# Optimization experiments

Hardware: AMD Instinct MI355X
Metric: run time of the kernel (lower is better)

Reference implementation:

```python
import jax, jax.numpy as jnp
import numpy as np

NUM_CODES = 128
BETA = 0.25


def conv1d(x, w, b):
    # x: (B, C, T), w: (O, I, K) torch layout, 'same' padding for k=3
    y = jax.lax.conv_general_dilated(x, w, window_strides=(1,), padding=[(1, 1)],
                                     dimension_numbers=('NCH', 'OIH', 'NCH'))
    return y + b[None, :, None]


def setup_inputs() -> dict:
    key = jax.random.key(0)
    ks = jax.random.split(key, 8)
    B, C, T, K = 16, 192, 8192, NUM_CODES
    fan = 1.0 / np.sqrt(C * 3)
    inp = {
        'x': jax.random.normal(ks[0], (B, C, T), jnp.float32),
        'enc_w1': jax.random.normal(ks[1], (C, C, 3), jnp.float32) * fan,
        'enc_b1': jnp.zeros((C,), jnp.float32),
        'enc_w2': jax.random.normal(ks[2], (C, C, 3), jnp.float32) * fan,
        'enc_b2': jnp.zeros((C,), jnp.float32),
        'emb': jax.random.normal(ks[3], (K, C), jnp.float32) * (1.0 / K),
        'dec_w1': jax.random.normal(ks[4], (C, C, 3), jnp.float32) * fan,
        'dec_b1': jnp.zeros((C,), jnp.float32),
        'dec_w2': jax.random.normal(ks[5], (C, C, 3), jnp.float32) * fan,
        'dec_b2': jnp.zeros((C,), jnp.float32),
        'dec_w3': jax.random.normal(ks[6], (C, C, 3), jnp.float32) * fan,
        'dec_b3': jnp.zeros((C,), jnp.float32),
    }
    return inp


def vector_quantize(z_e, emb):
    # z_e: (B, C, T) -> tokens (B*T, C)
    B, C, T = z_e.shape
    z = jnp.transpose(z_e, (0, 2, 1)).reshape(-1, C)          # (N, C)
    # squared distances ||z||^2 + ||e||^2 - 2 z.e
    d = (jnp.sum(z * z, axis=1, keepdims=True)
         + jnp.sum(emb * emb, axis=1)[None, :]
         - 2.0 * (z @ emb.T))                                  # (N, K)
    idx = jnp.argmin(d, axis=1)                                # (N,)
    z_q = emb[idx]                                             # (N, C) gather
    # loss = ||sg(z_q) - z||^2*... standard: codebook + beta*commitment
    loss = (jnp.mean((jax.lax.stop_gradient(z_q) - z) ** 2)
            + BETA * jnp.mean((z_q - jax.lax.stop_gradient(z)) ** 2))
    # perplexity of code usage
    n = z.shape[0]
    counts = jnp.zeros((emb.shape[0],), z.dtype).at[idx].add(1.0)
    probs = counts / n
    perplexity = jnp.exp(-jnp.sum(probs * jnp.log(probs + 1e-10)))
    # straight-through
    z_q = z + jax.lax.stop_gradient(z_q - z)
    z_q = jnp.transpose(z_q.reshape(B, T, C), (0, 2, 1))
    return loss, z_q, perplexity, idx


def reference(x, enc_w1, enc_b1, enc_w2, enc_b2, emb,
              dec_w1, dec_b1, dec_w2, dec_b2, dec_w3, dec_b3):
    # encoder: conv -> relu -> conv
    z_e = conv1d(jax.nn.relu(conv1d(x, enc_w1, enc_b1)), enc_w2, enc_b2)
    embedding_loss, z_q, perplexity, _ = vector_quantize(z_e, emb)
    # NOTE: source forward decodes z_e (not z_q) — reproduced faithfully
    h = jax.nn.relu(conv1d(z_e, dec_w1, dec_b1))
    h = jax.nn.relu(conv1d(h, dec_w2, dec_b2))
    x_hat = conv1d(h, dec_w3, dec_b3)
    return embedding_loss, x_hat, perplexity
```

## Files before the change

kernel.cpp:

```cpp
#include <hip/hip_runtime.h>
#include <hip/hip_bf16.h>
#include <stdint.h>

typedef short s16x8 __attribute__((ext_vector_type(8)));
typedef float f32x4 __attribute__((ext_vector_type(4)));
typedef unsigned int u32;
typedef unsigned short u16;

#define CCH 192
#define APITCH 200
#define NCODES 128
#define HALO 9
#define RPB 8216
#define LEAD 12
#define TOK 256
#define AROWS 274
#define CHS 16384

__device__ __forceinline__ u16 f2b(float f) {
  u32 u = __builtin_bit_cast(u32, f);
  u = (u + 0x7fffu + ((u >> 16) & 1u)) >> 16;
  return (u16)u;
}
__device__ __forceinline__ float b2f(u16 h) {
  return __builtin_bit_cast(float, ((u32)h) << 16);
}
__device__ __forceinline__ void gld16(const void* g, void* l) {
  __builtin_amdgcn_global_load_lds(
      (const __attribute__((address_space(1))) void*)g,
      (__attribute__((address_space(3))) void*)l, 16, 0, 0);
}

__global__ __launch_bounds__(256) void k_tin(const float* __restrict__ x, u16* __restrict__ xtp,
                                             int B, int T) {
  __shared__ float tile[32][36];
  int nt = T >> 5;
  int bid = blockIdx.x;
  int b = bid / (6 * nt);
  int rem = bid % (6 * nt);
  int cb = rem / nt, tb = rem % nt;
  int tid = threadIdx.x;
  {
    int c = tid >> 3, seg = tid & 7;
    const float* src = x + ((size_t)b * CCH + cb * 32 + c) * T + tb * 32 + seg * 4;
    float4 v = *(const float4*)src;
    tile[c][seg * 4 + 0] = v.x; tile[c][seg * 4 + 1] = v.y;
    tile[c][seg * 4 + 2] = v.z; tile[c][seg * 4 + 3] = v.w;
  }
  __syncthreads();
  {
    int t = tid >> 3, cs = tid & 7;
    u16* dst = xtp + ((size_t)(b * RPB + LEAD + tb * 32 + t)) * APITCH + cb * 32 + cs * 4;
    ushort4 o;
    o.x = f2b(tile[cs * 4 + 0][t]); o.y = f2b(tile[cs * 4 + 1][t]);
    o.z = f2b(tile[cs * 4 + 2][t]); o.w = f2b(tile[cs * 4 + 3][t]);
    *(ushort4*)dst = o;
  }
}

__global__ __launch_bounds__(256) void k_padz(u16* __restrict__ xtp) {
  int b = blockIdx.x;
  for (int i = threadIdx.x; i < 24 * 25; i += 256) {
    int r = i / 25, c = i - (i / 25) * 25;
    int row = (r < 12) ? r : (RPB - 12 + (r - 12));
    uint4 z = {0u, 0u, 0u, 0u};
    *(uint4*)((char*)xtp + ((size_t)(b * RPB + row)) * 400 + c * 16) = z;
  }
}

__global__ __launch_bounds__(256) void k_wconv(const float* __restrict__ w, u16* __restrict__ dst) {
  int i = blockIdx.x * 256 + threadIdx.x;
  if (i >= 3 * CCH * CCH) return;
  int cb = i / 18432;
  int r = i - cb * 18432;
  int k = r / 6144;
  int r2 = r - k * 6144;
  int o = r2 / 32, il = r2 - o * 32;
  dst[(size_t)(cb * 3 + k) * (CHS / 2) + (il >> 3) * 1536 + o * 8 + (il & 7)] =
      f2b(w[(o * CCH + cb * 32 + il) * 3 + k]);
}

__global__ __launch_bounds__(64) void k_emb(const float* __restrict__ emb, u16* __restrict__ embp,
                                            float* __restrict__ e2) {
  int code = blockIdx.x, lane = threadIdx.x;
  float s = 0.f;
  for (int j = lane * 3; j < lane * 3 + 3; ++j) {
    float v = emb[code * CCH + j];
    int cb = j >> 5, il = j & 31;
    embp[(size_t)cb * 4096 + (il >> 3) * 1024 + code * 8 + (il & 7)] = f2b(v);
    s += v * v;
  }
  #pragma unroll
  for (int m = 1; m < 64; m <<= 1) s += __shfl_xor(s, m, 64);
  if (lane == 0) e2[code] = s;
}

__global__ void k_zero(int* hist, double* dsum) {
  int t = threadIdx.x;
  if (t < NCODES) hist[t] = 0;
  if (t == 0) *dsum = 0.0;
}

__device__ __forceinline__ void issueW(const char* src, u16* dstb, int wv, int lane) {
  const char* s0 = src + wv * 2048 + lane * 16;
  char* d0 = (char*)dstb + wv * 2048 + lane * 16;
  gld16(s0, d0);
  gld16(s0 + 1024, d0 + 1024);
}
__device__ __forceinline__ void issueE(const char* src, u16* dstb, int tid) {
  gld16(src + tid * 16, (char*)dstb + tid * 16);
}

template<int F, int S, int M>
__device__ __forceinline__ void af_load(u32 aaddr, s16x8 (&a)[2][F]) {
  constexpr int cb = S / 3, k = S - 3 * (S / 3);
  constexpr int imm = (16 * M + k) * 400 + cb * 64;
  asm volatile("ds_read_b128 %0, %1 offset:%2" : "=v"(a[S & 1][M]) : "v"(aaddr), "i"(imm));
  if constexpr (M + 1 < F) af_load<F, S, M + 1>(aaddr, a);
}
template<int NF>
__device__ __forceinline__ void wf_load(u32 wq, s16x8 (&wf)[3]) {
  asm volatile("ds_read_b128 %0, %1 offset:%2" : "=v"(wf[NF]) : "v"(wq), "i"(NF * 256));
  if constexpr (NF + 1 < 3) wf_load<NF + 1>(wq, wf);
}

template<int G0, int F, int NEXT, int S>
__device__ __forceinline__ void cstep(const char* __restrict__ wtp, const char* __restrict__ embp,
                                      u16 (*wb)[8192], u32 aaddr, u32 wq0, u32 wq1,
                                      int wv, int lane, int tid,
                                      s16x8 (&a)[2][F], f32x4 (&acc)[F][3]) {
  asm volatile("s_waitcnt vmcnt(0)" ::: "memory");
  __builtin_amdgcn_sched_barrier(0);
  __builtin_amdgcn_s_barrier();
  if constexpr (S < 17) issueW(wtp + (size_t)(G0 + S + 1) * CHS, wb[(S + 1) & 1], wv, lane);
  else if constexpr (NEXT == 1) issueW(wtp + (size_t)(G0 + 18) * CHS, wb[0], wv, lane);
  else if constexpr (NEXT == 2) issueE(embp, wb[0], tid);
  if constexpr (S == 0) af_load<F, 0, 0>(aaddr, a);
  s16x8 wf[3];
  wf_load<0>((S & 1) ? wq1 : wq0, wf);
  if constexpr (S < 17) {
    af_load<F, S + 1, 0>(aaddr, a);
    if constexpr (F == 9) asm volatile("s_waitcnt lgkmcnt(9)" ::: "memory");
    else                  asm volatile("s_waitcnt lgkmcnt(8)" ::: "memory");
  } else {
    asm volatile("s_waitcnt lgkmcnt(0)" ::: "memory");
  }
  __builtin_amdgcn_sched_barrier(0);
  #pragma unroll
  for (int nf = 0; nf < 3; ++nf)
    #pragma unroll
    for (int m = 0; m < F; ++m)
      acc[m][nf] = __builtin_amdgcn_mfma_f32_16x16x32_bf16(a[S & 1][m], wf[nf], acc[m][nf], 0, 0, 0);
  if constexpr (S + 1 < 18)
    cstep<G0, F, NEXT, S + 1>(wtp, embp, wb, aaddr, wq0, wq1, wv, lane, tid, a, acc);
}

template<int G0, int F, int NEXT>
__device__ __forceinline__ void conv_phase(const char* __restrict__ wtp, const char* __restrict__ embp,
                                           u16 (*wb)[8192], u32 aaddr, u32 wq0, u32 wq1,
                                           int wv, int lane, int tid, f32x4 (&acc)[F][3]) {
  s16x8 a[2][F];
  cstep<G0, F, NEXT, 0>(wtp, embp, wb, aaddr, wq0, wq1, wv, lane, tid, a, acc);
}

template<int F, bool RELU>
__device__ __forceinline__ void writeback(u16* __restrict__ act, const f32x4 (&acc)[F][3],
                                          const float* bv, int oB, int lr, int lg, int rbase,
                                          int t0, int T, bool edge) {
  __builtin_amdgcn_s_barrier();
  if (!edge) {
    #pragma unroll
    for (int m = 0; m < F; ++m)
      #pragma unroll
      for (int nf = 0; nf < 3; ++nf) {
        int o = oB + nf * 16 + lr;
        #pragma unroll
        for (int r = 0; r < 4; ++r) {
          int row = rbase + 16 * m + lg * 4 + r;
          float v = acc[m][nf][r] + bv[nf];
          if (RELU) v = fmaxf(v, 0.f);
          act[row * APITCH + o] = f2b(v);
        }
      }
  } else {
    #pragma unroll
    for (int m = 0; m < F; ++m)
      #pragma unroll
      for (int nf = 0; nf < 3; ++nf) {
        int o = oB + nf * 16 + lr;
        #pragma unroll
        for (int r = 0; r < 4; ++r) {
          int row = rbase + 16 * m + lg * 4 + r;
          int tok = t0 - HALO + row;
          float v = acc[m][nf][r] + bv[nf];
          if (RELU) v = fmaxf(v, 0.f);
          if (tok < 0 || tok >= T) v = 0.f;
          act[row * APITCH + o] = f2b(v);
        }
      }
  }
  asm volatile("s_waitcnt lgkmcnt(0)" ::: "memory");
  __builtin_amdgcn_s_barrier();
}

__global__ __launch_bounds__(512, 1) void k_fused(
    const char* __restrict__ xtp, const char* __restrict__ wtp,
    const float* __restrict__ eb1, const float* __restrict__ eb2,
    const float* __restrict__ db1, const float* __restrict__ db2, const float* __restrict__ db3,
    const char* __restrict__ embp, const float* __restrict__ e2,
    int* __restrict__ hist, double* __restrict__ dsum,
    float* __restrict__ xhat, int T) {
  __shared__ __align__(16) u16 act[AROWS * APITCH];
  __shared__ __align__(16) u16 wb[2][8192];
  __shared__ int hs[NCODES];
  __shared__ float wsum[8];
  const int tid = threadIdx.x;
  const int wv = tid >> 6, lane = tid & 63, lr = lane & 15, lg = lane >> 4;
  const int nw = wv & 3, mw = wv >> 2;
  const int bid = blockIdx.x;
  const int b = bid >> 5, tile = bid & 31;
  const int t0 = tile * TOK;
  const bool edge = (tile == 0) || (tile == 31);
  const int oB = nw * 48;
  const int rbase = 1 + mw * 128;
  if (tid < NCODES) hs[tid] = 0;

  const u32 aaddr = (u32)(uintptr_t)act + (u32)(((rbase - 1 + lr) * APITCH + lg * 8) * 2);
  const u32 wq0 = (u32)(uintptr_t)wb[0] + (u32)((lg * 1536 + (oB + lr) * 8) * 2);
  const u32 wq1 = wq0 + 16384u;

  float bvv[5][3];
  #pragma unroll
  for (int nf = 0; nf < 3; ++nf) {
    int o = oB + nf * 16 + lr;
    bvv[0][nf] = eb1[o]; bvv[1][nf] = eb2[o];
    bvv[2][nf] = db1[o]; bvv[3][nf] = db2[o]; bvv[4][nf] = db3[o];
  }

  {
    const char* src = xtp + (size_t)(b * RPB + LEAD + t0 - HALO) * 400;
    #pragma unroll
    for (int s = 0; s < 14; ++s) {
      int c = tid + s * 512;
      if (c < AROWS * 25)
        gld16(src + (size_t)c * 16, (char*)act + (size_t)c * 16);
    }
  }
  issueW(wtp, wb[0], wv, lane);

  {
    f32x4 acc[9][3];
    #pragma unroll
    for (int m = 0; m < 9; ++m)
      #pragma unroll
      for (int n = 0; n < 3; ++n) acc[m][n] = f32x4{0.f, 0.f, 0.f, 0.f};
    conv_phase<0, 9, 1>(wtp, embp, wb, aaddr, wq0, wq1, wv, lane, tid, acc);
    writeback<9, true>(act, acc, bvv[0], oB, lr, lg, rbase, t0, T, edge);
  }
  {
    f32x4 acc[9][3];
    #pragma unroll
    for (int m = 0; m < 9; ++m)
      #pragma unroll
      for (int n = 0; n < 3; ++n) acc[m][n] = f32x4{0.f, 0.f, 0.f, 0.f};
    conv_phase<18, 9, 2>(wtp, embp, wb, aaddr, wq0, wq1, wv, lane, tid, acc);
    writeback<9, false>(act, acc, bvv[1], oB, lr, lg, rbase, t0, T, edge);
  }

  {
    f32x4 va0[8], va1[8];
    #pragma unroll
    for (int n = 0; n < 8; ++n) { va0[n] = f32x4{0.f,0.f,0.f,0.f}; va1[n] = f32x4{0.f,0.f,0.f,0.f}; }
    const int zr0 = 9 + wv * 32 + lr;
    #pragma unroll 2
    for (int s = 0; s < 6; ++s) {
      asm volatile("s_waitcnt vmcnt(0)" ::: "memory");
      __builtin_amdgcn_sched_barrier(0);
      __builtin_amdgcn_s_barrier();
      if (s < 5) issueE(embp + (s + 1) * 8192, wb[(s + 1) & 1], tid);
      else issueW(wtp + (size_t)36 * CHS, wb[0], wv, lane);
      const u16* eq = wb[s & 1] + lg * 1024 + lr * 8;
      s16x8 az0 = *(const s16x8*)(act + zr0 * APITCH + s * 32 + lg * 8);
      s16x8 az1 = *(const s16x8*)(act + (zr0 + 16) * APITCH + s * 32 + lg * 8);
      #pragma unroll
      for (int nf = 0; nf < 8; ++nf) {
        s16x8 ef = *(const s16x8*)(eq + nf * 128);
        va0[nf] = __builtin_amdgcn_mfma_f32_16x16x32_bf16(az0, ef, va0[nf], 0, 0, 0);
        va1[nf] = __builtin_amdgcn_mfma_f32_16x16x32_bf16(az1, ef, va1[nf], 0, 0, 0);
      }
    }
    float e2v[8];
    #pragma unroll
    for (int nf = 0; nf < 8; ++nf) e2v[nf] = e2[nf * 16 + lr];
    float dpart = 0.f;
    #pragma unroll
    for (int rg = 0; rg < 2; ++rg) {
      float z2 = 0.f;
      const u16* zr = act + (zr0 + rg * 16) * APITCH + lg * 48;
      #pragma unroll
      for (int j = 0; j < 48; j += 8) {
        s16x8 vv = *(const s16x8*)(zr + j);
        #pragma unroll
        for (int e = 0; e < 8; ++e) { float f = b2f((u16)vv[e]); z2 += f * f; }
      }
      z2 += __shfl_xor(z2, 16, 64);
      z2 += __shfl_xor(z2, 32, 64);
      float smin[4]; int imin[4];
      #pragma unroll
      for (int r = 0; r < 4; ++r) { smin[r] = 3.4e38f; imin[r] = 0; }
      #pragma unroll
      for (int nf = 0; nf < 8; ++nf) {
        int code = nf * 16 + lr;
        #pragma unroll
        for (int r = 0; r < 4; ++r) {
          float sc = e2v[nf] - 2.f * (rg ? va1[nf][r] : va0[nf][r]);
          if (sc < smin[r]) { smin[r] = sc; imin[r] = code; }
        }
      }
      #pragma unroll
      for (int m = 1; m < 16; m <<= 1) {
        #pragma unroll
        for (int r = 0; r < 4; ++r) {
          float so = __shfl_xor(smin[r], m, 64);
          int io = __shfl_xor(imin[r], m, 64);
          if (so < smin[r] || (so == smin[r] && io < imin[r])) { smin[r] = so; imin[r] = io; }
        }
      }
      #pragma unroll
      for (int r = 0; r < 4; ++r) {
        float z2t = __shfl(z2, lg * 4 + r, 64);
        if (lr == 0) {
          dpart += z2t + smin[r];
          atomicAdd(&hs[imin[r]], 1);
        }
      }
    }
    #pragma unroll
    for (int m = 1; m < 64; m <<= 1) dpart += __shfl_xor(dpart, m, 64);
    if (lane == 0) wsum[wv] = dpart;
    asm volatile("s_waitcnt lgkmcnt(0)" ::: "memory");
    __builtin_amdgcn_s_barrier();
    if (tid == 0) {
      double tot = 0.0;
      #pragma unroll
      for (int w = 0; w < 8; ++w) tot += (double)wsum[w];
      atomicAdd(dsum, tot);
    }
    if (tid < NCODES && hs[tid] > 0) atomicAdd(&hist[tid], hs[tid]);
  }

  {
    f32x4 acc[9][3];
    #pragma unroll
    for (int m = 0; m < 9; ++m)
      #pragma unroll
      for (int n = 0; n < 3; ++n) acc[m][n] = f32x4{0.f, 0.f, 0.f, 0.f};
    conv_phase<36, 9, 1>(wtp, embp, wb, aaddr, wq0, wq1, wv, lane, tid, acc);
    writeback<9, true>(act, acc, bvv[2], oB, lr, lg, rbase, t0, T, edge);
  }
  {
    f32x4 acc[9][3];
    #pragma unroll
    for (int m = 0; m < 9; ++m)
      #pragma unroll
      for (int n = 0; n < 3; ++n) acc[m][n] = f32x4{0.f, 0.f, 0.f, 0.f};
    conv_phase<54, 9, 1>(wtp, embp, wb, aaddr, wq0, wq1, wv, lane, tid, acc);
    writeback<9, true>(act, acc, bvv[3], oB, lr, lg, rbase, t0, T, edge);
  }

  f32x4 acc5[8][3];
  #pragma unroll
  for (int m = 0; m < 8; ++m)
    #pragma unroll
    for (int n = 0; n < 3; ++n) acc5[m][n] = f32x4{0.f, 0.f, 0.f, 0.f};
  {
    const u32 aaddr3 = (u32)(uintptr_t)act + (u32)(((8 + mw * 128 + lr) * APITCH + lg * 8) * 2);
    conv_phase<72, 8, 0>(wtp, embp, wb, aaddr3, wq0, wq1, wv, lane, tid, acc5);
  }

  float* ft = (float*)act;
  float* dstb = xhat + (size_t)b * CCH * T + t0;
  #pragma unroll
  for (int p = 0; p < 2; ++p) {
    __builtin_amdgcn_s_barrier();
    if ((nw >> 1) == p) {
      #pragma unroll
      for (int m = 0; m < 8; ++m)
        #pragma unroll
        for (int nf = 0; nf < 3; ++nf) {
          int o = (nw & 1) * 48 + nf * 16 + lr;
          #pragma unroll
          for (int r = 0; r < 4; ++r) {
            int tl = mw * 128 + 16 * m + lg * 4 + r;
            ft[o * 260 + tl] = acc5[m][nf][r] + bvv[4][nf];
          }
        }
    }
    asm volatile("s_waitcnt lgkmcnt(0)" ::: "memory");
    __builtin_amdgcn_s_barrier();
    #pragma unroll
    for (int i = 0; i < 48; ++i) {
      int s = tid + i * 512;
      int o = s >> 8, tl = s & 255;
      dstb[(size_t)(o + p * 96) * T + tl] = ft[o * 260 + tl];
    }
  }
}

__global__ __launch_bounds__(128) void k_fin(const int* __restrict__ hist,
                                             const double* __restrict__ dsum,
                                             float* __restrict__ out, int N, int ppos) {
  __shared__ float H[NCODES];
  int t = threadIdx.x;
  float p = (float)hist[t] / (float)N;
  H[t] = p * logf(p + 1e-10f);
  __syncthreads();
  if (t == 0) {
    float s = 0.f;
    for (int i = 0; i < NCODES; ++i) s += H[i];
    out[ppos] = expf(-s);
    out[0] = (float)(1.25 * (*dsum) / ((double)N * (double)CCH));
  }
}

extern "C" void kernel_launch(void* const* d_in, const int* in_sizes, int n_in,
                              void* d_out, int out_size, void* d_ws, size_t ws_size,
                              hipStream_t stream) {
  const int B = 16, T = 8192, N = B * T;
  const float* x   = (const float*)d_in[0];
  const float* ew1 = (const float*)d_in[1];
  const float* eb1 = (const float*)d_in[2];
  const float* ew2 = (const float*)d_in[3];
  const float* eb2 = (const float*)d_in[4];
  const float* emb = (const float*)d_in[5];
  const float* dw1 = (const float*)d_in[6];
  const float* db1 = (const float*)d_in[7];
  const float* dw2 = (const float*)d_in[8];
  const float* db2 = (const float*)d_in[9];
  const float* dw3 = (const float*)d_in[10];
  const float* db3 = (const float*)d_in[11];

  char* ws = (char*)d_ws;
  char*  xtp  = ws;
  char*  wtp  = ws + 52583424;
  char*  embp = ws + 54057984;
  float* e2   = (float*)(ws + 54107136);
  int*   hist = (int*)(ws + 54107648);
  double* dsum = (double*)(ws + 54108160);

  const int wblocks = (3 * CCH * CCH + 255) / 256;
  const int TCH = 18 * (CHS / 2);
  k_wconv<<<wblocks, 256, 0, stream>>>(ew1, (u16*)wtp);
  k_wconv<<<wblocks, 256, 0, stream>>>(ew2, (u16*)wtp + TCH);
  k_wconv<<<wblocks, 256, 0, stream>>>(dw1, (u16*)wtp + 2 * TCH);
  k_wconv<<<wblocks, 256, 0, stream>>>(dw2, (u16*)wtp + 3 * TCH);
  k_wconv<<<wblocks, 256, 0, stream>>>(dw3, (u16*)wtp + 4 * TCH);
  k_emb<<<NCODES, 64, 0, stream>>>(emb, (u16*)embp, e2);
  k_zero<<<1, 256, 0, stream>>>(hist, dsum);
  k_padz<<<B, 256, 0, stream>>>((u16*)xtp);
  k_tin<<<B * 6 * (T / 32), 256, 0, stream>>>(x, (u16*)xtp, B, T);

  k_fused<<<B * (T / TOK), 512, 0, stream>>>(xtp, wtp, eb1, eb2, db1, db2, db3,
                                             embp, e2, hist, dsum, (float*)d_out + 1, T);
  k_fin<<<1, 128, 0, stream>>>(hist, dsum, (float*)d_out, N, out_size - 1);
}
```

Before: 235.3 us.

## Halve fused kernel to 4 waves with wider per-wave output tiles

The fused conv+VQ kernel drops from 8 waves per 512-thread block to 4 waves per 256-thread block. Each wave now covers 96 output channels instead of 48, so it reuses each A fragment across twice as many MFMAs. The VQ stage has each wave handle 64 token rows and load its codebook fragments once per step. Tile staging loops and the output copy loop are scaled to the smaller thread count. The cost is far more accumulator registers (9x6 f32x4 per wave) and fewer waves to hide LDS and global latency, which risks spills or stalls.

```diff
diff --git a/kernel.cpp b/kernel.cpp
--- a/kernel.cpp
+++ b/kernel.cpp
@@ -102,13 +102,16 @@
 }
 
 __device__ __forceinline__ void issueW(const char* src, u16* dstb, int wv, int lane) {
+  const char* s0 = src + wv * 4096 + lane * 16;
+  char* d0 = (char*)dstb + wv * 4096 + lane * 16;
+  #pragma unroll
+  for (int j = 0; j < 4; ++j) gld16(s0 + j * 1024, d0 + j * 1024);
+}
+__device__ __forceinline__ void issueE(const char* src, u16* dstb, int wv, int lane) {
   const char* s0 = src + wv * 2048 + lane * 16;
   char* d0 = (char*)dstb + wv * 2048 + lane * 16;
   gld16(s0, d0);
   gld16(s0 + 1024, d0 + 1024);
-}
-__device__ __forceinline__ void issueE(const char* src, u16* dstb, int tid) {
-  gld16(src + tid * 16, (char*)dstb + tid * 16);
 }
 
 template<int F, int S, int M>
@@ -118,26 +121,26 @@
   asm volatile("ds_read_b128 %0, %1 offset:%2" : "=v"(a[S & 1][M]) : "v"(aaddr), "i"(imm));
   if constexpr (M + 1 < F) af_load<F, S, M + 1>(aaddr, a);
 }
-template<int NF>
-__device__ __forceinline__ void wf_load(u32 wq, s16x8 (&wf)[3]) {
-  asm volatile("ds_read_b128 %0, %1 offset:%2" : "=v"(wf[NF]) : "v"(wq), "i"(NF * 256));
-  if constexpr (NF + 1 < 3) wf_load<NF + 1>(wq, wf);
-}
-
-template<int G0, int F, int NEXT, int S>
+template<int NF, int J>
+__device__ __forceinline__ void wf_load(u32 wq, s16x8 (&wf)[NF]) {
+  asm volatile("ds_read_b128 %0, %1 offset:%2" : "=v"(wf[J]) : "v"(wq), "i"(J * 256));
+  if constexpr (J + 1 < NF) wf_load<NF, J + 1>(wq, wf);
+}
+
+template<int G0, int F, int NF, int NEXT, int S>
 __device__ __forceinline__ void cstep(const char* __restrict__ wtp, const char* __restrict__ embp,
                                       u16 (*wb)[8192], u32 aaddr, u32 wq0, u32 wq1,
-                                      int wv, int lane, int tid,
-                                      s16x8 (&a)[2][F], f32x4 (&acc)[F][3]) {
+                                      int wv, int lane,
+                                      s16x8 (&a)[2][F], f32x4 (&acc)[F][NF]) {
   asm volatile("s_waitcnt vmcnt(0)" ::: "memory");
   __builtin_amdgcn_sched_barrier(0);
   __builtin_amdgcn_s_barrier();
   if constexpr (S < 17) issueW(wtp + (size_t)(G0 + S + 1) * CHS, wb[(S + 1) & 1], wv, lane);
   else if constexpr (NEXT == 1) issueW(wtp + (size_t)(G0 + 18) * CHS, wb[0], wv, lane);
-  else if constexpr (NEXT == 2) issueE(embp, wb[0], tid);
+  else if constexpr (NEXT == 2) issueE(embp, wb[0], wv, lane);
   if constexpr (S == 0) af_load<F, 0, 0>(aaddr, a);
-  s16x8 wf[3];
-  wf_load<0>((S & 1) ? wq1 : wq0, wf);
+  s16x8 wf[NF];
+  wf_load<NF, 0>((S & 1) ? wq1 : wq0, wf);
   if constexpr (S < 17) {
     af_load<F, S + 1, 0>(aaddr, a);
     if constexpr (F == 9) asm volatile("s_waitcnt lgkmcnt(9)" ::: "memory");
@@ -147,32 +150,36 @@
   }
   __builtin_amdgcn_sched_barrier(0);
   #pragma unroll
-  for (int nf = 0; nf < 3; ++nf)
+  for (int nf = 0; nf < NF; ++nf)
     #pragma unroll
     for (int m = 0; m < F; ++m)
       acc[m][nf] = __builtin_amdgcn_mfma_f32_16x16x32_bf16(a[S & 1][m], wf[nf], acc[m][nf], 0, 0, 0);
   if constexpr (S + 1 < 18)
-    cstep<G0, F, NEXT, S + 1>(wtp, embp, wb, aaddr, wq0, wq1, wv, lane, tid, a, acc);
-}
-
-template<int G0, int F, int NEXT>
+    cstep<G0, F, NF, NEXT, S + 1>(wtp, embp, wb, aaddr, wq0, wq1, wv, lane, a, acc);
+}
+
+template<int G0, int F, int NF, int NEXT>
 __device__ __forceinline__ void conv_phase(const char* __restrict__ wtp, const char* __restrict__ embp,
                                            u16 (*wb)[8192], u32 aaddr, u32 wq0, u32 wq1,
-                                           int wv, int lane, int tid, f32x4 (&acc)[F][3]) {
+                                           int wv, int lane, f32x4 (&acc)[F][NF]) {
   s16x8 a[2][F];
-  cstep<G0, F, NEXT, 0>(wtp, embp, wb, aaddr, wq0, wq1, wv, lane, tid, a, acc);
-}
-
-template<int F, bool RELU>
-__device__ __forceinline__ void writeback(u16* __restrict__ act, const f32x4 (&acc)[F][3],
-                                          const float* bv, int oB, int lr, int lg, int rbase,
+  cstep<G0, F, NF, NEXT, 0>(wtp, embp, wb, aaddr, wq0, wq1, wv, lane, a, acc);
+}
+
+template<int F, int NF, bool RELU>
+__device__ __forceinline__ void writeback(u16* __restrict__ act, const f32x4 (&acc)[F][NF],
+                                          const float* __restrict__ bias,
+                                          int oB, int lr, int lg, int rbase,
                                           int t0, int T, bool edge) {
+  float bv[NF];
+  #pragma unroll
+  for (int nf = 0; nf < NF; ++nf) bv[nf] = bias[oB + nf * 16 + lr];
   __builtin_amdgcn_s_barrier();
   if (!edge) {
     #pragma unroll
     for (int m = 0; m < F; ++m)
       #pragma unroll
-      for (int nf = 0; nf < 3; ++nf) {
+      for (int nf = 0; nf < NF; ++nf) {
         int o = oB + nf * 16 + lr;
         #pragma unroll
         for (int r = 0; r < 4; ++r) {
@@ -186,7 +193,7 @@
     #pragma unroll
     for (int m = 0; m < F; ++m)
       #pragma unroll
-      for (int nf = 0; nf < 3; ++nf) {
+      for (int nf = 0; nf < NF; ++nf) {
         int o = oB + nf * 16 + lr;
         #pragma unroll
         for (int r = 0; r < 4; ++r) {
@@ -203,7 +210,7 @@
   __builtin_amdgcn_s_barrier();
 }
 
-__global__ __launch_bounds__(512, 1) void k_fused(
+__global__ __launch_bounds__(256, 1) void k_fused(
     const char* __restrict__ xtp, const char* __restrict__ wtp,
     const float* __restrict__ eb1, const float* __restrict__ eb2,
     const float* __restrict__ db1, const float* __restrict__ db2, const float* __restrict__ db3,
@@ -213,15 +220,15 @@
   __shared__ __align__(16) u16 act[AROWS * APITCH];
   __shared__ __align__(16) u16 wb[2][8192];
   __shared__ int hs[NCODES];
-  __shared__ float wsum[8];
+  __shared__ float wsum[4];
   const int tid = threadIdx.x;
   const int wv = tid >> 6, lane = tid & 63, lr = lane & 15, lg = lane >> 4;
-  const int nw = wv & 3, mw = wv >> 2;
+  const int nw = wv & 1, mw = wv >> 1;
   const int bid = blockIdx.x;
   const int b = bid >> 5, tile = bid & 31;
   const int t0 = tile * TOK;
   const bool edge = (tile == 0) || (tile == 31);
-  const int oB = nw * 48;
+  const int oB = nw * 96;
   const int rbase = 1 + mw * 128;
   if (tid < NCODES) hs[tid] = 0;
 
@@ -229,19 +236,11 @@
   const u32 wq0 = (u32)(uintptr_t)wb[0] + (u32)((lg * 1536 + (oB + lr) * 8) * 2);
   const u32 wq1 = wq0 + 16384u;
 
-  float bvv[5][3];
-  #pragma unroll
-  for (int nf = 0; nf < 3; ++nf) {
-    int o = oB + nf * 16 + lr;
-    bvv[0][nf] = eb1[o]; bvv[1][nf] = eb2[o];
-    bvv[2][nf] = db1[o]; bvv[3][nf] = db2[o]; bvv[4][nf] = db3[o];
-  }
-
   {
     const char* src = xtp + (size_t)(b * RPB + LEAD + t0 - HALO) * 400;
     #pragma unroll
-    for (int s = 0; s < 14; ++s) {
-      int c = tid + s * 512;
+    for (int s = 0; s < 27; ++s) {
+      int c = tid + s * 256;
       if (c < AROWS * 25)
         gld16(src + (size_t)c * 16, (char*)act + (size_t)c * 16);
     }
@@ -249,44 +248,48 @@
   issueW(wtp, wb[0], wv, lane);
 
   {
-    f32x4 acc[9][3];
+    f32x4 acc[9][6];
     #pragma unroll
     for (int m = 0; m < 9; ++m)
       #pragma unroll
-      for (int n = 0; n < 3; ++n) acc[m][n] = f32x4{0.f, 0.f, 0.f, 0.f};
-    conv_phase<0, 9, 1>(wtp, embp, wb, aaddr, wq0, wq1, wv, lane, tid, acc);
-    writeback<9, true>(act, acc, bvv[0], oB, lr, lg, rbase, t0, T, edge);
-  }
-  {
-    f32x4 acc[9][3];
+      for (int n = 0; n < 6; ++n) acc[m][n] = f32x4{0.f, 0.f, 0.f, 0.f};
+    conv_phase<0, 9, 6, 1>(wtp, embp, wb, aaddr, wq0, wq1, wv, lane, acc);
+    writeback<9, 6, true>(act, acc, eb1, oB, lr, lg, rbase, t0, T, edge);
+  }
+  {
+    f32x4 acc[9][6];
     #pragma unroll
     for (int m = 0; m < 9; ++m)
       #pragma unroll
-      for (int n = 0; n < 3; ++n) acc[m][n] = f32x4{0.f, 0.f, 0.f, 0.f};
-    conv_phase<18, 9, 2>(wtp, embp, wb, aaddr, wq0, wq1, wv, lane, tid, acc);
-    writeback<9, false>(act, acc, bvv[1], oB, lr, lg, rbase, t0, T, edge);
-  }
-
-  {
-    f32x4 va0[8], va1[8];
-    #pragma unroll
-    for (int n = 0; n < 8; ++n) { va0[n] = f32x4{0.f,0.f,0.f,0.f}; va1[n] = f32x4{0.f,0.f,0.f,0.f}; }
-    const int zr0 = 9 + wv * 32 + lr;
+      for (int n = 0; n < 6; ++n) acc[m][n] = f32x4{0.f, 0.f, 0.f, 0.f};
+    conv_phase<18, 9, 6, 2>(wtp, embp, wb, aaddr, wq0, wq1, wv, lane, acc);
+    writeback<9, 6, false>(act, acc, eb2, oB, lr, lg, rbase, t0, T, edge);
+  }
+
+  {
+    f32x4 va[4][8];
+    #pragma unroll
+    for (int rg = 0; rg < 4; ++rg)
+      #pragma unroll
+      for (int n = 0; n < 8; ++n) va[rg][n] = f32x4{0.f, 0.f, 0.f, 0.f};
+    const int zr0 = HALO + wv * 64 + lr;
     #pragma unroll 2
     for (int s = 0; s < 6; ++s) {
       asm volatile("s_waitcnt vmcnt(0)" ::: "memory");
       __builtin_amdgcn_sched_barrier(0);
       __builtin_amdgcn_s_barrier();
-      if (s < 5) issueE(embp + (s + 1) * 8192, wb[(s + 1) & 1], tid);
+      if (s < 5) issueE(embp + (s + 1) * 8192, wb[(s + 1) & 1], wv, lane);
       else issueW(wtp + (size_t)36 * CHS, wb[0], wv, lane);
       const u16* eq = wb[s & 1] + lg * 1024 + lr * 8;
-      s16x8 az0 = *(const s16x8*)(act + zr0 * APITCH + s * 32 + lg * 8);
-      s16x8 az1 = *(const s16x8*)(act + (zr0 + 16) * APITCH + s * 32 + lg * 8);
-      #pragma unroll
-      for (int nf = 0; nf < 8; ++nf) {
-        s16x8 ef = *(const s16x8*)(eq + nf * 128);
-        va0[nf] = __builtin_amdgcn_mfma_f32_16x16x32_bf16(az0, ef, va0[nf], 0, 0, 0);
-        va1[nf] = __builtin_amdgcn_mfma_f32_16x16x32_bf16(az1, ef, va1[nf], 0, 0, 0);
+      s16x8 eqf[8];
+      #pragma unroll
+      for (int nf = 0; nf < 8; ++nf) eqf[nf] = *(const s16x8*)(eq + nf * 128);
+      #pragma unroll
+      for (int rg = 0; rg < 4; ++rg) {
+        s16x8 az = *(const s16x8*)(act + (zr0 + rg * 16) * APITCH + s * 32 + lg * 8);
+        #pragma unroll
+        for (int nf = 0; nf < 8; ++nf)
+          va[rg][nf] = __builtin_amdgcn_mfma_f32_16x16x32_bf16(az, eqf[nf], va[rg][nf], 0, 0, 0);
       }
     }
     float e2v[8];
@@ -294,7 +297,7 @@
     for (int nf = 0; nf < 8; ++nf) e2v[nf] = e2[nf * 16 + lr];
     float dpart = 0.f;
     #pragma unroll
-    for (int rg = 0; rg < 2; ++rg) {
+    for (int rg = 0; rg < 4; ++rg) {
       float z2 = 0.f;
       const u16* zr = act + (zr0 + rg * 16) * APITCH + lg * 48;
       #pragma unroll
@@ -313,7 +316,7 @@
         int code = nf * 16 + lr;
         #pragma unroll
         for (int r = 0; r < 4; ++r) {
-          float sc = e2v[nf] - 2.f * (rg ? va1[nf][r] : va0[nf][r]);
+          float sc = e2v[nf] - 2.f * va[rg][nf][r];
           if (sc < smin[r]) { smin[r] = sc; imin[r] = code; }
         }
       }
@@ -343,64 +346,67 @@
     if (tid == 0) {
       double tot = 0.0;
       #pragma unroll
-      for (int w = 0; w < 8; ++w) tot += (double)wsum[w];
+      for (int w = 0; w < 4; ++w) tot += (double)wsum[w];
       atomicAdd(dsum, tot);
     }
     if (tid < NCODES && hs[tid] > 0) atomicAdd(&hist[tid], hs[tid]);
   }
 
   {
-    f32x4 acc[9][3];
+    f32x4 acc[9][6];
     #pragma unroll
     for (int m = 0; m < 9; ++m)
       #pragma unroll
-      for (int n = 0; n < 3; ++n) acc[m][n] = f32x4{0.f, 0.f, 0.f, 0.f};
-    conv_phase<36, 9, 1>(wtp, embp, wb, aaddr, wq0, wq1, wv, lane, tid, acc);
-    writeback<9, true>(act, acc, bvv[2], oB, lr, lg, rbase, t0, T, edge);
-  }
-  {
-    f32x4 acc[9][3];
+      for (int n = 0; n < 6; ++n) acc[m][n] = f32x4{0.f, 0.f, 0.f, 0.f};
+    conv_phase<36, 9, 6, 1>(wtp, embp, wb, aaddr, wq0, wq1, wv, lane, acc);
+    writeback<9, 6, true>(act, acc, db1, oB, lr, lg, rbase, t0, T, edge);
+  }
+  {
+    f32x4 acc[9][6];
     #pragma unroll
     for (int m = 0; m < 9; ++m)
       #pragma unroll
-      for (int n = 0; n < 3; ++n) acc[m][n] = f32x4{0.f, 0.f, 0.f, 0.f};
-    conv_phase<54, 9, 1>(wtp, embp, wb, aaddr, wq0, wq1, wv, lane, tid, acc);
-    writeback<9, true>(act, acc, bvv[3], oB, lr, lg, rbase, t0, T, edge);
-  }
-
-  f32x4 acc5[8][3];
+      for (int n = 0; n < 6; ++n) acc[m][n] = f32x4{0.f, 0.f, 0.f, 0.f};
+    conv_phase<54, 9, 6, 1>(wtp, embp, wb, aaddr, wq0, wq1, wv, lane, acc);
+    writeback<9, 6, true>(act, acc, db2, oB, lr, lg, rbase, t0, T, edge);
+  }
+
+  f32x4 acc5[8][6];
   #pragma unroll
   for (int m = 0; m < 8; ++m)
     #pragma unroll
-    for (int n = 0; n < 3; ++n) acc5[m][n] = f32x4{0.f, 0.f, 0.f, 0.f};
+    for (int n = 0; n < 6; ++n) acc5[m][n] = f32x4{0.f, 0.f, 0.f, 0.f};
   {
     const u32 aaddr3 = (u32)(uintptr_t)act + (u32)(((8 + mw * 128 + lr) * APITCH + lg * 8) * 2);
-    conv_phase<72, 8, 0>(wtp, embp, wb, aaddr3, wq0, wq1, wv, lane, tid, acc5);
-  }
+    conv_phase<72, 8, 6, 0>(wtp, embp, wb, aaddr3, wq0, wq1, wv, lane, acc5);
+  }
+  float bv3[6];
+  #pragma unroll
+  for (int nf = 0; nf < 6; ++nf) bv3[nf] = db3[oB + nf * 16 + lr];
 
   float* ft = (float*)act;
   float* dstb = xhat + (size_t)b * CCH * T + t0;
   #pragma unroll
   for (int p = 0; p < 2; ++p) {
     __builtin_amdgcn_s_barrier();
-    if ((nw >> 1) == p) {
+    if (nw == p) {
       #pragma unroll
       for (int m = 0; m < 8; ++m)
         #pragma unroll
-        for (int nf = 0; nf < 3; ++nf) {
-          int o = (nw & 1) * 48 + nf * 16 + lr;
+        for (int nf = 0; nf < 6; ++nf) {
+          int o = nf * 16 + lr;
           #pragma unroll
           for (int r = 0; r < 4; ++r) {
             int tl = mw * 128 + 16 * m + lg * 4 + r;
-            ft[o * 260 + tl] = acc5[m][nf][r] + bvv[4][nf];
+            ft[o * 260 + tl] = acc5[m][nf][r] + bv3[nf];
           }
         }
     }
     asm volatile("s_waitcnt lgkmcnt(0)" ::: "memory");
     __builtin_amdgcn_s_barrier();
     #pragma unroll
-    for (int i = 0; i < 48; ++i) {
-      int s = tid + i * 512;
+    for (int i = 0; i < 96; ++i) {
+      int s = tid + i * 256;
       int o = s >> 8, tl = s & 255;
       dstb[(size_t)(o + p * 96) * T + tl] = ft[o * 260 + tl];
     }
@@ -460,7 +466,7 @@
   k_padz<<<B, 256, 0, stream>>>((u16*)xtp);
   k_tin<<<B * 6 * (T / 32), 256, 0, stream>>>(x, (u16*)xtp, B, T);
 
-  k_fused<<<B * (T / TOK), 512, 0, stream>>>(xtp, wtp, eb1, eb2, db1, db2, db3,
+  k_fused<<<B * (T / TOK), 256, 0, stream>>>(xtp, wtp, eb1, eb2, db1, db2, db3,
                                              embp, e2, hist, dsum, (float*)d_out + 1, T);
   k_fin<<<1, 128, 0, stream>>>(hist, dsum, (float*)d_out, N, out_size - 1);
 }
```

Result: slower. 285.9 us (+21.5%).
